# Kernel tuning notes

Hardware: AMD Instinct MI355X
Metric: run time of the kernel (lower is better)

The kernel has to match this reference:

```python
import jax, jax.numpy as jnp
import numpy as np

N = 2_000_000
C_IN = 32
C_OUT = 64
K_TAPS = 8  # kernel_size=2 in 3D -> 2^3 taps
EPS = 1e-5


def setup_inputs() -> dict:
    key = jax.random.key(0)
    k1, k2, k3, k4, k5 = jax.random.split(key, 5)
    features = jax.random.normal(k1, (N, C_IN), dtype=jnp.float32)
    gamma = jax.random.uniform(k2, (C_IN,), dtype=jnp.float32)
    beta = jnp.zeros((C_IN,), dtype=jnp.float32)
    weight = jax.random.normal(k3, (K_TAPS, C_IN, C_OUT), dtype=jnp.float32)
    # kernel-map: output segment id and kernel-tap id per input point
    out_index = jax.random.randint(k4, (N,), 0, N, dtype=jnp.int64)
    offset_index = jax.random.randint(k5, (N,), 0, K_TAPS, dtype=jnp.int64)
    return {
        "features": features,
        "gamma": gamma,
        "beta": beta,
        "weight": weight,
        "out_index": out_index,
        "offset_index": offset_index,
    }


def reference(features, gamma, beta, weight, out_index, offset_index):
    # BatchNorm over all active points (training-mode batch stats, biased var)
    mean = jnp.mean(features, axis=0)
    var = jnp.var(features, axis=0)
    x = (features - mean) * jax.lax.rsqrt(var + EPS) * gamma + beta
    # ReLU
    x = jnp.maximum(x, 0.0)
    # Sparse conv, stride == kernel_size: each point hits one output cell via one tap.
    # Loop over the fixed 8 kernel taps; mask, dense matmul, scatter-add.
    out = jnp.zeros((N, C_OUT), dtype=features.dtype)
    for tap in range(K_TAPS):
        xt = jnp.where((offset_index == tap)[:, None], x, 0.0)  # [N, C_in]
        contrib = xt @ weight[tap]  # [N, C_out]
        out = out + jax.ops.segment_sum(contrib, out_index, num_segments=N)
    return out
```

## Files before the change

### kernel.cpp

```cpp
#include <hip/hip_runtime.h>
#include <stdint.h>

#define EPS 1e-5f

typedef __attribute__((ext_vector_type(8))) __bf16 bf16x8;
typedef __attribute__((ext_vector_type(8))) unsigned short ushort8;
typedef __attribute__((ext_vector_type(4))) float f32x4;

__device__ __forceinline__ unsigned short f2bf(float f) {
    union { float f; unsigned u; } c; c.f = f;
    unsigned r = c.u + 0x7fffu + ((c.u >> 16) & 1u);
    return (unsigned short)(r >> 16);
}

__global__ void stats_kernel(const float* __restrict__ f, float* __restrict__ ws, int n) {
    __shared__ float s_sum[32];
    __shared__ float s_sq[32];
    int tid = threadIdx.x;
    if (tid < 32) { s_sum[tid] = 0.f; s_sq[tid] = 0.f; }
    __syncthreads();
    int c = tid & 31;
    int g = tid >> 5;
    float sum = 0.f, sq = 0.f;
    for (int r = blockIdx.x * 8 + g; r < n; r += gridDim.x * 8) {
        float v = f[(size_t)r * 32 + c];
        sum += v; sq += v * v;
    }
    atomicAdd(&s_sum[c], sum);
    atomicAdd(&s_sq[c], sq);
    __syncthreads();
    if (tid < 32) {
        atomicAdd(&ws[tid],      s_sum[tid]);
        atomicAdd(&ws[32 + tid], s_sq[tid]);
    }
}

__global__ void finalize_kernel(const float* __restrict__ gamma, const float* __restrict__ beta,
                                float* __restrict__ ws, int n) {
    int c = threadIdx.x;
    if (c < 32) {
        float inv_n = 1.f / (float)n;
        float mean = ws[c] * inv_n;
        float var  = ws[32 + c] * inv_n - mean * mean;
        float scale = gamma[c] * rsqrtf(var + EPS);
        ws[64 + c] = scale;
        ws[96 + c] = beta[c] - mean * scale;
    }
}

__global__ __launch_bounds__(256, 2) void spconv_kernel(
    const float* __restrict__ feat, const float* __restrict__ weight,
    const int* __restrict__ out_idx, const int* __restrict__ off_idx,
    const float* __restrict__ ws, float* __restrict__ out, int n)
{
    const int lane = threadIdx.x & 63;
    const int m    = lane & 15;
    const int quad = lane >> 4;
    const int wave   = blockIdx.x * (blockDim.x >> 6) + (threadIdx.x >> 6);
    const int nwaves = gridDim.x * (blockDim.x >> 6);

    float scl[8], sft[8];
    #pragma unroll
    for (int j = 0; j < 8; ++j) {
        int k = quad * 8 + j;
        scl[j] = ws[64 + k];
        sft[j] = ws[96 + k];
    }

    ushort8 wf[8][4];
    #pragma unroll
    for (int t = 0; t < 8; ++t) {
        #pragma unroll
        for (int cb = 0; cb < 4; ++cb) {
            ushort8 v;
            #pragma unroll
            for (int j = 0; j < 8; ++j) {
                int k = quad * 8 + j;
                v[j] = f2bf(weight[((size_t)t * 32 + k) * 64 + cb * 16 + m]);
            }
            wf[t][cb] = v;
        }
    }

    const ushort8 zz = {0, 0, 0, 0, 0, 0, 0, 0};
    const int ntiles = (n + 15) >> 4;

    for (int tile = wave; tile < ntiles; tile += nwaves) {
        const int p_base = tile << 4;
        const int p  = p_base + m;
        const int pc = p < n ? p : n - 1;

        const f32x4* fp = (const f32x4*)(feat + (size_t)pc * 32 + quad * 8);
        f32x4 x0 = fp[0];
        f32x4 x1 = fp[1];

        ushort8 af;
        #pragma unroll
        for (int j = 0; j < 4; ++j)
            af[j] = f2bf(fmaxf(x0[j] * scl[j] + sft[j], 0.f));
        #pragma unroll
        for (int j = 0; j < 4; ++j)
            af[4 + j] = f2bf(fmaxf(x1[j] * scl[4 + j] + sft[4 + j], 0.f));

        const int tap = (p < n) ? off_idx[p] : -1;

        f32x4 acc[4];
        #pragma unroll
        for (int cb = 0; cb < 4; ++cb) acc[cb] = (f32x4){0.f, 0.f, 0.f, 0.f};

        #pragma unroll
        for (int t = 0; t < 8; ++t) {
            ushort8 am = (tap == t) ? af : zz;
            bf16x8 a = __builtin_bit_cast(bf16x8, am);
            #pragma unroll
            for (int cb = 0; cb < 4; ++cb) {
                acc[cb] = __builtin_amdgcn_mfma_f32_16x16x32_bf16(
                    a, __builtin_bit_cast(bf16x8, wf[t][cb]), acc[cb], 0, 0, 0);
            }
        }

        int o[4]; bool ok[4];
        #pragma unroll
        for (int i = 0; i < 4; ++i) {
            int pr = p_base + quad * 4 + i;
            ok[i] = pr < n;
            o[i]  = ok[i] ? out_idx[pr] : 0;
        }
        #pragma unroll
        for (int cb = 0; cb < 4; ++cb) {
            #pragma unroll
            for (int i = 0; i < 4; ++i) {
                if (ok[i])
                    atomicAdd(out + (size_t)o[i] * 64 + cb * 16 + m, acc[cb][i]);
            }
        }
    }
}

extern "C" void kernel_launch(void* const* d_in, const int* in_sizes, int n_in,
                              void* d_out, int out_size, void* d_ws, size_t ws_size,
                              hipStream_t stream) {
    const float* features  = (const float*)d_in[0];
    const float* gamma     = (const float*)d_in[1];
    const float* beta      = (const float*)d_in[2];
    const float* weight    = (const float*)d_in[3];
    const int*   out_index = (const int*)d_in[4];
    const int*   off_index = (const int*)d_in[5];
    float* out = (float*)d_out;
    float* ws  = (float*)d_ws;
    const int n = in_sizes[0] / 32;

    hipMemsetAsync(d_out, 0, (size_t)out_size * sizeof(float), stream);
    hipMemsetAsync(d_ws, 0, 64 * sizeof(float), stream);

    stats_kernel<<<2048, 256, 0, stream>>>(features, ws, n);
    finalize_kernel<<<1, 64, 0, stream>>>(gamma, beta, ws, n);
    spconv_kernel<<<1024, 256, 0, stream>>>(features, weight, out_index, off_index,
                                            ws, out, n);
}
```

Baseline: 1.142 ms.

## Replace atomic scatter-add with counting-sort CSR gather and direct output writes

Builds a histogram of output indices, computes an exclusive scan, and scatters point ids into a CSR ordering. Each output row then gathers its contributing points and runs the MFMA conv per segment. The full output is written once with plain stores, so the separate output memset and the float atomics go away. In exchange it adds a histogram, a three-pass scan and a scatter pass with integer atomics. Segment lengths are uneven and the feature reads become random gathers. A fallback path keeps the atomic version when the workspace is too small.

```diff
diff --git a/kernel.cpp b/kernel.cpp
--- a/kernel.cpp
+++ b/kernel.cpp
@@ -2,10 +2,12 @@
 #include <stdint.h>
 
 #define EPS 1e-5f
+#define NPB 2048
 
 typedef __attribute__((ext_vector_type(8))) __bf16 bf16x8;
 typedef __attribute__((ext_vector_type(8))) unsigned short ushort8;
 typedef __attribute__((ext_vector_type(4))) float f32x4;
+typedef __attribute__((ext_vector_type(4))) int i32x4;
 
 __device__ __forceinline__ unsigned short f2bf(float f) {
     union { float f; unsigned u; } c; c.f = f;
@@ -13,7 +15,9 @@
     return (unsigned short)(r >> 16);
 }
 
-__global__ void stats_kernel(const float* __restrict__ f, float* __restrict__ ws, int n) {
+__global__ void stats_hist_kernel(const float* __restrict__ f, const int* __restrict__ out_idx,
+                                  float* __restrict__ wsf, int* __restrict__ cnt,
+                                  int n, int do_hist) {
     __shared__ float s_sum[32];
     __shared__ float s_sq[32];
     int tid = threadIdx.x;
@@ -25,33 +29,111 @@
     for (int r = blockIdx.x * 8 + g; r < n; r += gridDim.x * 8) {
         float v = f[(size_t)r * 32 + c];
         sum += v; sq += v * v;
+        if (do_hist && c == 0) atomicAdd(&cnt[out_idx[r]], 1);
     }
     atomicAdd(&s_sum[c], sum);
     atomicAdd(&s_sq[c], sq);
     __syncthreads();
     if (tid < 32) {
-        atomicAdd(&ws[tid],      s_sum[tid]);
-        atomicAdd(&ws[32 + tid], s_sq[tid]);
+        atomicAdd(&wsf[tid],      s_sum[tid]);
+        atomicAdd(&wsf[32 + tid], s_sq[tid]);
     }
 }
 
 __global__ void finalize_kernel(const float* __restrict__ gamma, const float* __restrict__ beta,
-                                float* __restrict__ ws, int n) {
+                                float* __restrict__ wsf, int n) {
     int c = threadIdx.x;
     if (c < 32) {
         float inv_n = 1.f / (float)n;
-        float mean = ws[c] * inv_n;
-        float var  = ws[32 + c] * inv_n - mean * mean;
+        float mean = wsf[c] * inv_n;
+        float var  = wsf[32 + c] * inv_n - mean * mean;
         float scale = gamma[c] * rsqrtf(var + EPS);
-        ws[64 + c] = scale;
-        ws[96 + c] = beta[c] - mean * scale;
-    }
-}
-
-__global__ __launch_bounds__(256, 2) void spconv_kernel(
+        wsf[64 + c] = scale;
+        wsf[96 + c] = beta[c] - mean * scale;
+    }
+}
+
+__global__ void scan1_kernel(const int* __restrict__ cnt, int* __restrict__ offs,
+                             int* __restrict__ partials, int n) {
+    __shared__ int s[256];
+    int tid = threadIdx.x;
+    int base = blockIdx.x * NPB + tid * 8;
+    int v[8];
+    if (base + 8 <= n) {
+        i32x4 a = *(const i32x4*)(cnt + base);
+        i32x4 b = *(const i32x4*)(cnt + base + 4);
+        #pragma unroll
+        for (int i = 0; i < 4; ++i) { v[i] = a[i]; v[4 + i] = b[i]; }
+    } else {
+        #pragma unroll
+        for (int i = 0; i < 8; ++i) v[i] = (base + i < n) ? cnt[base + i] : 0;
+    }
+    int sum = 0;
+    #pragma unroll
+    for (int i = 0; i < 8; ++i) sum += v[i];
+    s[tid] = sum; __syncthreads();
+    for (int d = 1; d < 256; d <<= 1) {
+        int t = (tid >= d) ? s[tid - d] : 0;
+        __syncthreads();
+        s[tid] += t;
+        __syncthreads();
+    }
+    int run = s[tid] - sum;
+    #pragma unroll
+    for (int i = 0; i < 8; ++i) {
+        if (base + i < n) offs[base + i] = run;
+        run += v[i];
+    }
+    if (tid == 0) partials[blockIdx.x] = s[255];
+}
+
+__global__ void scan2_kernel(int* __restrict__ partials, int nparts) {
+    __shared__ int s[1024];
+    int tid = threadIdx.x;
+    int v = (tid < nparts) ? partials[tid] : 0;
+    s[tid] = v; __syncthreads();
+    for (int d = 1; d < 1024; d <<= 1) {
+        int t = (tid >= d) ? s[tid - d] : 0;
+        __syncthreads();
+        s[tid] += t;
+        __syncthreads();
+    }
+    if (tid < nparts) partials[tid] = s[tid] - v;
+}
+
+__global__ void scan3_kernel(int* __restrict__ offs, const int* __restrict__ partials, int n) {
+    int tid = threadIdx.x;
+    int add = partials[blockIdx.x];
+    int base = blockIdx.x * NPB + tid * 8;
+    if (base + 8 <= n) {
+        i32x4 a = *(i32x4*)(offs + base);
+        i32x4 b = *(i32x4*)(offs + base + 4);
+        #pragma unroll
+        for (int i = 0; i < 4; ++i) { a[i] += add; b[i] += add; }
+        *(i32x4*)(offs + base) = a;
+        *(i32x4*)(offs + base + 4) = b;
+    } else {
+        #pragma unroll
+        for (int i = 0; i < 8; ++i) if (base + i < n) offs[base + i] += add;
+    }
+}
+
+__global__ void scatter_kernel(const int* __restrict__ out_idx, int* __restrict__ offs,
+                               int* __restrict__ order, int n) {
+    int p = blockIdx.x * blockDim.x + threadIdx.x;
+    int stride = gridDim.x * blockDim.x;
+    for (; p < n; p += stride) {
+        int o = out_idx[p];
+        int pos = atomicAdd(&offs[o], 1);
+        order[pos] = p;
+    }
+}
+
+__global__ __launch_bounds__(256) void gather_kernel(
     const float* __restrict__ feat, const float* __restrict__ weight,
-    const int* __restrict__ out_idx, const int* __restrict__ off_idx,
-    const float* __restrict__ ws, float* __restrict__ out, int n)
+    const int* __restrict__ off_idx, const int* __restrict__ order,
+    const int* __restrict__ offs, const float* __restrict__ wsf,
+    float* __restrict__ out, int n)
 {
     const int lane = threadIdx.x & 63;
     const int m    = lane & 15;
@@ -63,8 +145,8 @@
     #pragma unroll
     for (int j = 0; j < 8; ++j) {
         int k = quad * 8 + j;
-        scl[j] = ws[64 + k];
-        sft[j] = ws[96 + k];
+        scl[j] = wsf[64 + k];
+        sft[j] = wsf[96 + k];
     }
 
     ushort8 wf[8][4];
@@ -83,55 +165,145 @@
     }
 
     const ushort8 zz = {0, 0, 0, 0, 0, 0, 0, 0};
+    const int ngroups = (n + 15) >> 4;
+
+    for (int g = wave; g < ngroups; g += nwaves) {
+        const int o_base = g << 4;
+        const int o_m = o_base + m;
+        int start = 0, end = 0;
+        if (o_m < n) {
+            end = offs[o_m];
+            start = (o_m > 0) ? offs[o_m - 1] : 0;
+        }
+        const int len = end - start;
+        int lmax = len;
+        #pragma unroll
+        for (int d = 1; d <= 8; d <<= 1)
+            lmax = max(lmax, __shfl_xor(lmax, d));
+
+        f32x4 acc[4];
+        #pragma unroll
+        for (int cb = 0; cb < 4; ++cb) acc[cb] = (f32x4){0.f, 0.f, 0.f, 0.f};
+
+        int p_next = (len > 0) ? order[start] : 0;
+        for (int r = 0; r < lmax; ++r) {
+            const bool act = r < len;
+            const int p = p_next;
+            p_next = (r + 1 < len) ? order[start + r + 1] : 0;
+            const int tap = act ? off_idx[p] : -1;
+
+            f32x4 x0 = (f32x4){0.f, 0.f, 0.f, 0.f};
+            f32x4 x1 = (f32x4){0.f, 0.f, 0.f, 0.f};
+            if (act) {
+                const f32x4* fp = (const f32x4*)(feat + (size_t)p * 32 + quad * 8);
+                x0 = fp[0];
+                x1 = fp[1];
+            }
+            ushort8 af;
+            #pragma unroll
+            for (int j = 0; j < 4; ++j)
+                af[j] = f2bf(fmaxf(x0[j] * scl[j] + sft[j], 0.f));
+            #pragma unroll
+            for (int j = 0; j < 4; ++j)
+                af[4 + j] = f2bf(fmaxf(x1[j] * scl[4 + j] + sft[4 + j], 0.f));
+
+            #pragma unroll
+            for (int t = 0; t < 8; ++t) {
+                ushort8 am = (tap == t) ? af : zz;
+                bf16x8 a = __builtin_bit_cast(bf16x8, am);
+                #pragma unroll
+                for (int cb = 0; cb < 4; ++cb) {
+                    acc[cb] = __builtin_amdgcn_mfma_f32_16x16x32_bf16(
+                        a, __builtin_bit_cast(bf16x8, wf[t][cb]), acc[cb], 0, 0, 0);
+                }
+            }
+        }
+
+        #pragma unroll
+        for (int i = 0; i < 4; ++i) {
+            int o = o_base + quad * 4 + i;
+            if (o < n) {
+                #pragma unroll
+                for (int cb = 0; cb < 4; ++cb)
+                    out[(size_t)o * 64 + cb * 16 + m] = acc[cb][i];
+            }
+        }
+    }
+}
+
+__global__ void fill_zero_kernel(float* __restrict__ p, size_t n4) {
+    size_t i = (size_t)blockIdx.x * blockDim.x + threadIdx.x;
+    size_t stride = (size_t)gridDim.x * blockDim.x;
+    f32x4 z = (f32x4){0.f, 0.f, 0.f, 0.f};
+    for (; i < n4; i += stride) ((f32x4*)p)[i] = z;
+}
+
+__global__ __launch_bounds__(256) void spconv_kernel(
+    const float* __restrict__ feat, const float* __restrict__ weight,
+    const int* __restrict__ out_idx, const int* __restrict__ off_idx,
+    const float* __restrict__ wsf, float* __restrict__ out, int n)
+{
+    const int lane = threadIdx.x & 63;
+    const int m    = lane & 15;
+    const int quad = lane >> 4;
+    const int wave   = blockIdx.x * (blockDim.x >> 6) + (threadIdx.x >> 6);
+    const int nwaves = gridDim.x * (blockDim.x >> 6);
+
+    float scl[8], sft[8];
+    #pragma unroll
+    for (int j = 0; j < 8; ++j) {
+        int k = quad * 8 + j;
+        scl[j] = wsf[64 + k];
+        sft[j] = wsf[96 + k];
+    }
+    ushort8 wf[8][4];
+    #pragma unroll
+    for (int t = 0; t < 8; ++t) {
+        #pragma unroll
+        for (int cb = 0; cb < 4; ++cb) {
+            ushort8 v;
+            #pragma unroll
+            for (int j = 0; j < 8; ++j)
+                v[j] = f2bf(weight[((size_t)t * 32 + quad * 8 + j) * 64 + cb * 16 + m]);
+            wf[t][cb] = v;
+        }
+    }
+
+    const ushort8 zz = {0, 0, 0, 0, 0, 0, 0, 0};
     const int ntiles = (n + 15) >> 4;
-
     for (int tile = wave; tile < ntiles; tile += nwaves) {
         const int p_base = tile << 4;
         const int p  = p_base + m;
         const int pc = p < n ? p : n - 1;
-
         const f32x4* fp = (const f32x4*)(feat + (size_t)pc * 32 + quad * 8);
         f32x4 x0 = fp[0];
         f32x4 x1 = fp[1];
-
         ushort8 af;
         #pragma unroll
-        for (int j = 0; j < 4; ++j)
-            af[j] = f2bf(fmaxf(x0[j] * scl[j] + sft[j], 0.f));
-        #pragma unroll
-        for (int j = 0; j < 4; ++j)
-            af[4 + j] = f2bf(fmaxf(x1[j] * scl[4 + j] + sft[4 + j], 0.f));
-
+        for (int j = 0; j < 4; ++j) af[j] = f2bf(fmaxf(x0[j] * scl[j] + sft[j], 0.f));
+        #pragma unroll
+        for (int j = 0; j < 4; ++j) af[4 + j] = f2bf(fmaxf(x1[j] * scl[4 + j] + sft[4 + j], 0.f));
         const int tap = (p < n) ? off_idx[p] : -1;
-
         f32x4 acc[4];
         #pragma unroll
         for (int cb = 0; cb < 4; ++cb) acc[cb] = (f32x4){0.f, 0.f, 0.f, 0.f};
-
         #pragma unroll
         for (int t = 0; t < 8; ++t) {
             ushort8 am = (tap == t) ? af : zz;
             bf16x8 a = __builtin_bit_cast(bf16x8, am);
             #pragma unroll
-            for (int cb = 0; cb < 4; ++cb) {
+            for (int cb = 0; cb < 4; ++cb)
                 acc[cb] = __builtin_amdgcn_mfma_f32_16x16x32_bf16(
                     a, __builtin_bit_cast(bf16x8, wf[t][cb]), acc[cb], 0, 0, 0);
-            }
-        }
-
-        int o[4]; bool ok[4];
+        }
         #pragma unroll
         for (int i = 0; i < 4; ++i) {
             int pr = p_base + quad * 4 + i;
-            ok[i] = pr < n;
-            o[i]  = ok[i] ? out_idx[pr] : 0;
-        }
-        #pragma unroll
-        for (int cb = 0; cb < 4; ++cb) {
-            #pragma unroll
-            for (int i = 0; i < 4; ++i) {
-                if (ok[i])
-                    atomicAdd(out + (size_t)o[i] * 64 + cb * 16 + m, acc[cb][i]);
+            if (pr < n) {
+                int o = out_idx[pr];
+                #pragma unroll
+                for (int cb = 0; cb < 4; ++cb)
+                    atomicAdd(out + (size_t)o * 64 + cb * 16 + m, acc[cb][i]);
             }
         }
     }
@@ -147,14 +319,35 @@
     const int*   out_index = (const int*)d_in[4];
     const int*   off_index = (const int*)d_in[5];
     float* out = (float*)d_out;
-    float* ws  = (float*)d_ws;
     const int n = in_sizes[0] / 32;
 
-    hipMemsetAsync(d_out, 0, (size_t)out_size * sizeof(float), stream);
-    hipMemsetAsync(d_ws, 0, 64 * sizeof(float), stream);
-
-    stats_kernel<<<2048, 256, 0, stream>>>(features, ws, n);
-    finalize_kernel<<<1, 64, 0, stream>>>(gamma, beta, ws, n);
-    spconv_kernel<<<1024, 256, 0, stream>>>(features, weight, out_index, off_index,
-                                            ws, out, n);
-}
+    const int nparts = (n + NPB - 1) / NPB;
+    const int NPAD   = nparts * NPB;
+
+    float* wsf      = (float*)d_ws;
+    int*   cnt      = (int*)((char*)d_ws + 1024);
+    int*   offs     = cnt + NPAD;
+    int*   order    = offs + NPAD;
+    int*   partials = order + NPAD;
+    size_t needed   = 1024 + ((size_t)3 * NPAD + 1024) * sizeof(int);
+
+    if (ws_size >= needed && nparts <= 1024) {
+        hipMemsetAsync(d_ws, 0, 1024, stream);
+        hipMemsetAsync(cnt, 0, (size_t)n * sizeof(int), stream);
+        stats_hist_kernel<<<2048, 256, 0, stream>>>(features, out_index, wsf, cnt, n, 1);
+        finalize_kernel<<<1, 64, 0, stream>>>(gamma, beta, wsf, n);
+        scan1_kernel<<<nparts, 256, 0, stream>>>(cnt, offs, partials, n);
+        scan2_kernel<<<1, 1024, 0, stream>>>(partials, nparts);
+        scan3_kernel<<<nparts, 256, 0, stream>>>(offs, partials, n);
+        scatter_kernel<<<2048, 256, 0, stream>>>(out_index, offs, order, n);
+        gather_kernel<<<4096, 256, 0, stream>>>(features, weight, off_index, order,
+                                                offs, wsf, out, n);
+    } else {
+        hipMemsetAsync(d_ws, 0, 1024, stream);
+        fill_zero_kernel<<<2048, 256, 0, stream>>>(out, (size_t)out_size / 4);
+        stats_hist_kernel<<<2048, 256, 0, stream>>>(features, out_index, wsf, nullptr, n, 0);
+        finalize_kernel<<<1, 64, 0, stream>>>(gamma, beta, wsf, n);
+        spconv_kernel<<<4096, 256, 0, stream>>>(features, weight, out_index, off_index,
+                                                wsf, out, n);
+    }
+}
```

Measured after the change: 1.322 ms. 15.7% more time.
